# Kernel tuning notes

Measured on AMD Instinct MI355X. Metric: run time of the kernel, lower is better.

Reference implementation:

```python
import jax, jax.numpy as jnp
import numpy as np

H = 0.01      # RK4 step size (parameter.h)
LAM = 1.0     # stage-cost gate penalty
R_COST = 0.1  # scalar control cost R
WMIN, WMAX = -0.01, 0.01  # disturbance range
B, N_STATES, T_STEPS = 8192, 2, 2048

# substituted plant dynamics (parameter.x1_dot / parameter.x2_dot)
def _x1_dot(x1, x2, u):
    return -2.0 * x1 + x2 + u

def _x2_dot(x1, x2, u):
    return x1 - 2.0 * x2 + u

def _rk4_step(x, u):
    # Faithful to RungeKutta.f: k2 == k3 (both evaluated at x2 + h/2)
    x1, x2 = x[0], x[1]
    k1 = jnp.stack([_x1_dot(x1, x2, u), _x2_dot(x1, x2, u)])
    k2 = jnp.stack([_x1_dot(x1, x2 + H / 2, u), _x2_dot(x1, x2 + H / 2, u)])
    k4 = jnp.stack([_x1_dot(x1, x2 + H, u), _x2_dot(x1, x2 + H, u)])
    return x + H * (k1 + 4.0 * k2 + k4) / 6.0  # (k1+2k2+2k3+k4)/6 with k3=k2


def setup_inputs() -> dict:
    key = jax.random.key(0)
    kw, kK, kL, kM, kMo = jax.random.split(key, 5)
    w = jax.random.uniform(kw, (B, N_STATES, T_STEPS), dtype=jnp.float32,
                           minval=WMIN, maxval=WMAX)
    K = 0.1 * jax.random.normal(kK, (1, N_STATES), dtype=jnp.float32)
    L = 0.05 * jax.random.normal(kL, (2 * N_STATES, 2 * N_STATES), dtype=jnp.float32)
    M = 0.05 * jax.random.normal(kM, (1, 2 * N_STATES), dtype=jnp.float32)
    Mo = 0.05 * jax.random.normal(kMo, (1, 1), dtype=jnp.float32)
    return {"w": w, "K": K, "L": L, "M": M, "Mo": Mo}


def reference(w, K, L, M, Mo):
    # w: (B, N, T) disturbances; returns per-sample trajectory cost J, shape (B,)
    Bsz, N, T = w.shape
    dt = w.dtype
    Q = jnp.eye(N, dtype=dt)
    Qf = 10.0 * jnp.eye(N, dtype=dt)
    x0 = jnp.zeros((N,), dtype=dt).at[0].set(1.0)  # xf = 0
    steps = jnp.arange(T)

    def traj_cost(w_b):  # w_b: (N, T)
        def step(carry, inp):
            x, x_hat = carry          # each (N,)
            w_t, i = inp
            z = jnp.concatenate([x, x_hat])            # phi input (2N,)
            phi = z @ L @ z + M[0] @ z + Mo[0, 0]
            delta = jnp.where(i == 0, jnp.asarray(1.0, dt), jax.nn.sigmoid(phi))
            x_hat_n = jnp.where(i == 0, x_hat, delta * x + (1.0 - delta) * x_hat)
            u = K[0] @ x_hat_n                         # control from gated estimate
            x_next = _rk4_step(x, u) + w_t
            u_s = K[0] @ x                             # J uses K @ x[:,i]
            sc = x @ Q @ x + R_COST * u_s * u_s + LAM * delta
            return (x_next, x_hat_n), sc

        (x_T, _), scs = jax.lax.scan(step, (x0, x0), (w_b.T, steps))
        return jnp.sum(scs[: T - 1]) + x_T @ Qf @ x_T

    return jax.vmap(traj_cost)(w)
```

## Files before the change

### kernel.cpp

```cpp
#include <hip/hip_runtime.h>


#define T_STEPS 2048
#define BATCH   8192

__device__ __forceinline__ float swapf(float v) {
    return __int_as_float(__builtin_amdgcn_update_dpp(
        0, __float_as_int(v), 0xB1, 0xF, 0xF, true));
}

__global__ __launch_bounds__(64, 1) void cstr_kernel(
    const float* __restrict__ w,
    const float* __restrict__ K,
    const float* __restrict__ L,
    const float* __restrict__ M,
    const float* __restrict__ Mo,
    float* __restrict__ out)
{
    const int lane = threadIdx.x;
    const int p = lane & 1;
    const int s = blockIdx.x * 32 + (lane >> 1);

    const float k1c = K[0], k2c = K[1];
    const float s11 = L[0];
    const float s12 = L[1] + L[4];
    const float s13 = L[2] + L[8];
    const float s14 = L[3] + L[12];
    const float s22 = L[5];
    const float s23 = L[6] + L[9];
    const float s24 = L[7] + L[13];
    const float s33 = L[10];
    const float s34 = L[11] + L[14];
    const float s44 = L[15];
    const float m1 = M[0], m2 = M[1], m3 = M[2], m4 = M[3];
    const float c0 = Mo[0];

    constexpr float Hs = 0.01f;
    constexpr float Ad = 1.0f - 2.0f * Hs;
    constexpr float Rc = 0.1f;
    constexpr float SC = -1.44269504088896340736f;

    float P1, P2, P3, P4, P5, P6, P7, P8;
    if (p == 0) { P1 = s11; P2 = s12; P3 = s13; P4 = s14; P5 = m1; P6 = s33; P7 = s34; P8 = m3; }
    else        { P1 = s22; P2 = 0.f; P3 = s24; P4 = s23; P5 = m2; P6 = s44; P7 = 0.f; P8 = m4; }
    P1 *= SC; P2 *= SC; P3 *= SC; P4 *= SC; P5 *= SC; P6 *= SC; P7 *= SC; P8 *= SC;
    const float P9 = 0.5f * c0 * SC;

    const float kown = p ? k2c : k1c;
    const float koth = p ? k1c : k2c;
    const float hk   = Hs * kown;
    const float Cown = p ? (-Hs * Hs) : (0.5f * Hs * Hs);

    float x   = p ? 0.0f : 1.0f;
    float xh  = x;
    float accO = 0.0f;
    float accD = 0.0f;

    auto step = [&](float wv, bool first, bool cost) {
        float xo  = swapf(x);
        float xho = swapf(xh);
        float d;
        if (first) {
            d = 1.0f;
        } else {
            float t  = fmaf(P2, xo, fmaf(P1, x, P5));
            t        = fmaf(P3, xh, t);
            t        = fmaf(P4, xho, t);
            float u2 = fmaf(P7, xho, fmaf(P6, xh, P8));
            float part = fmaf(xh, u2, fmaf(x, t, P9));
            float e  = __builtin_amdgcn_exp2f(part + swapf(part));
            d        = __builtin_amdgcn_rcpf(1.0f + e);
            xh       = fmaf(d, x - xh, xh);
        }
        if (cost) {
            float us = fmaf(kown, x, koth * xo);
            accO = fmaf(x, x, accO);
            accD = fmaf(Rc * us, us, accD);
            accD += d;
        }
        float pown = hk * xh;
        float hu   = pown + swapf(pown);
        x = fmaf(Ad, x, fmaf(Hs, xo, wv + Cown)) + hu;
    };

    auto chunk = [&](const float4* buf, bool first, bool lastchunk) {
        #pragma unroll
        for (int q = 0; q < 4; ++q) {
            float4 a = buf[q];
            step(a.x, first && (q == 0), true);
            step(a.y, false, true);
            step(a.z, false, true);
            step(a.w, false, !(lastchunk && (q == 3)));
        }
    };

    const float4* r = reinterpret_cast<const float4*>(
        w + ((size_t)s * 2 + p) * T_STEPS);

    float4 Abuf[4], Bbuf[4];
    #pragma unroll
    for (int q = 0; q < 4; ++q) Abuf[q] = r[q];
    #pragma unroll
    for (int q = 0; q < 4; ++q) Bbuf[q] = r[4 + q];

    chunk(Abuf, true, false);

    for (int i = 0; i < 63; ++i) {
        const float4* pa = r + (size_t)(2 + 2 * i) * 4;
        #pragma unroll
        for (int q = 0; q < 4; ++q) Abuf[q] = pa[q];
        chunk(Bbuf, false, false);
        const float4* pb = r + (size_t)(3 + 2 * i) * 4;
        #pragma unroll
        for (int q = 0; q < 4; ++q) Bbuf[q] = pb[q];
        chunk(Abuf, false, false);
    }
    chunk(Bbuf, false, true);

    accO = fmaf(10.0f * x, x, accO);
    float J = accO + swapf(accO) + accD;
    if (p == 0) out[s] = J;
}

extern "C" void kernel_launch(void* const* d_in, const int* in_sizes, int n_in,
                              void* d_out, int out_size, void* d_ws, size_t ws_size,
                              hipStream_t stream) {
    const float* w  = (const float*)d_in[0];
    const float* K  = (const float*)d_in[1];
    const float* L  = (const float*)d_in[2];
    const float* M  = (const float*)d_in[3];
    const float* Mo = (const float*)d_in[4];
    float* out = (float*)d_out;

    hipLaunchKernelGGL(cstr_kernel, dim3(BATCH * 2 / 64), dim3(64), 0, stream,
                       w, K, L, M, Mo, out);
}
```

Measured before the change: 301.5 us.

## Express next gate logit as quadratic in gate to shorten serial chain

Rewrites the per-step recurrence so the next step's sigmoid argument is a quadratic in the current gate value d. Its coefficients are computed from pre-gate state in parallel with the exp/rcp, and the estimate-error terms dx/dxo are tracked explicitly. The control-cost term is moved out of the loop by accumulating x·x and x·xo and combining them with K once at the end. This aims to cut latency on the strictly serial per-sample dependency chain, at the cost of more FMAs and swaps per step and slightly different floating-point rounding.

Result: slower. 323.7 us (+7.4%).

```diff
diff --git a/kernel.cpp b/kernel.cpp
--- a/kernel.cpp
+++ b/kernel.cpp
@@ -44,43 +44,61 @@
     if (p == 0) { P1 = s11; P2 = s12; P3 = s13; P4 = s14; P5 = m1; P6 = s33; P7 = s34; P8 = m3; }
     else        { P1 = s22; P2 = 0.f; P3 = s24; P4 = s23; P5 = m2; P6 = s44; P7 = 0.f; P8 = m4; }
     P1 *= SC; P2 *= SC; P3 *= SC; P4 *= SC; P5 *= SC; P6 *= SC; P7 *= SC; P8 *= SC;
-    const float P9 = 0.5f * c0 * SC;
+    const float P9  = 0.5f * c0 * SC;
+    const float P12 = P1 + P2;
 
     const float kown = p ? k2c : k1c;
-    const float koth = p ? k1c : k2c;
-    const float hk   = Hs * kown;
+    const float Hk   = Hs * kown;
     const float Cown = p ? (-Hs * Hs) : (0.5f * Hs * Hs);
 
-    float x   = p ? 0.0f : 1.0f;
-    float xh  = x;
+    float x  = p ? 0.0f : 1.0f;
+    float h  = x;
+    float xo = p ? 1.0f : 0.0f;
+    float ho = xo;
+    float dx = 0.0f, dxo = 0.0f;
+    float hu0c = Hs * k1c + Cown;
+    float phi  = 0.0f;
     float accO = 0.0f;
+    float accXY = 0.0f;
     float accD = 0.0f;
 
     auto step = [&](float wv, bool first, bool cost) {
-        float xo  = swapf(x);
-        float xho = swapf(xh);
         float d;
-        if (first) {
-            d = 1.0f;
-        } else {
-            float t  = fmaf(P2, xo, fmaf(P1, x, P5));
-            t        = fmaf(P3, xh, t);
-            t        = fmaf(P4, xho, t);
-            float u2 = fmaf(P7, xho, fmaf(P6, xh, P8));
-            float part = fmaf(xh, u2, fmaf(x, t, P9));
-            float e  = __builtin_amdgcn_exp2f(part + swapf(part));
-            d        = __builtin_amdgcn_rcpf(1.0f + e);
-            xh       = fmaf(d, x - xh, xh);
-        }
+        float E = 0.0f;
+        if (!first) E = __builtin_amdgcn_exp2f(phi);
+
+        float gp  = Hk * dx;
+        float g   = gp + swapf(gp);
+        float wck = wv + hu0c;
+        float q   = fmaf(Ad, x, fmaf(Hs, xo, wck));
+        float qo  = swapf(q);
+        float t0  = fmaf(P4, ho, fmaf(P3, h, fmaf(P2, qo, fmaf(P1, q, P5))));
+        float t1  = fmaf(P12, g, fmaf(P3, dx, P4 * dxo));
+        float u0  = fmaf(P7, ho, fmaf(P6, h, P8));
+        float u1  = fmaf(P7, dxo, P6 * dx);
+        float pA  = fmaf(q, t0, fmaf(h, u0, P9));
+        float pB  = fmaf(q, t1, fmaf(g, t0, fmaf(h, u1, dx * u0)));
+        float pC  = fmaf(g, t1, dx * u1);
+        float Aq  = pA + swapf(pA);
+        float Bq  = pB + swapf(pB);
+        float Cq  = pC + swapf(pC);
+
+        if (first) d = 1.0f;
+        else       d = __builtin_amdgcn_rcpf(1.0f + E);
+
         if (cost) {
-            float us = fmaf(kown, x, koth * xo);
-            accO = fmaf(x, x, accO);
-            accD = fmaf(Rc * us, us, accD);
+            accO  = fmaf(x, x, accO);
+            accXY = fmaf(x, xo, accXY);
             accD += d;
         }
-        float pown = hk * xh;
-        float hu   = pown + swapf(pown);
-        x = fmaf(Ad, x, fmaf(Hs, xo, wv + Cown)) + hu;
+        phi = fmaf(d, fmaf(Cq, d, Bq), Aq);
+        x    = fmaf(d, g, q);
+        xo   = fmaf(d, g, qo);
+        h    = fmaf(d, dx, h);
+        ho   = fmaf(d, dxo, ho);
+        hu0c = fmaf(d, g, hu0c);
+        dx   = x - h;
+        dxo  = xo - ho;
     };
 
     auto chunk = [&](const float4* buf, bool first, bool lastchunk) {
@@ -117,8 +135,11 @@
     }
     chunk(Bbuf, false, true);
 
-    accO = fmaf(10.0f * x, x, accO);
-    float J = accO + swapf(accO) + accD;
+    float tt  = fmaf(kown * kown, accO, (k1c * k2c) * accXY);
+    float us2 = tt + swapf(tt);
+    float qq  = accO + swapf(accO);
+    float term = 10.0f * fmaf(x, x, xo * xo);
+    float J = qq + fmaf(Rc, us2, accD + term);
     if (p == 0) out[s] = J;
 }
 
```
